# Kernel optimization log

Measured on AMD Instinct MI355X. Metric: run time of the kernel, lower is better.

## Reference

```python
import jax, jax.numpy as jnp
import numpy as np
from jax.scipy.linalg import expm

B, S, D_H, D_C = 8, 1024, 64, 3

def setup_inputs() -> dict:
    key = jax.random.key(0)
    k1, k2, k3 = jax.random.split(key, 3)
    x = jax.random.normal(k1, (B, S, D_H), dtype=jnp.float32)
    r_grid = jax.random.uniform(k2, (B, S, D_C), dtype=jnp.float32)
    L_param = jax.random.normal(k3, (D_C, D_H, D_H), dtype=jnp.float32)
    P_sp = jnp.eye(D_H, dtype=jnp.float32)  # allow_mixing=False -> identity buffer
    return {"x": x, "r_grid": r_grid, "L_param": L_param, "P_sp": P_sp}

def reference(x, r_grid, L_param, P_sp):
    # skew-symmetrize each generator: L_k <- 0.5*(L_k - L_k^T)
    L_skew = 0.5 * (L_param - jnp.swapaxes(L_param, -1, -2))      # [d_c, d_h, d_h]
    # A_r[b,s] = sum_k r_grid[b,s,k] * L_skew[k]
    A_r = jnp.einsum('bsk,kij->bsij', r_grid, L_skew)             # [B, S, d_h, d_h]
    # batched matrix exponential over leading dims
    R_r = expm(A_r)                                               # [B, S, d_h, d_h]
    R_eff = R_r @ P_sp                                            # [B, S, d_h, d_h]
    x_out = jnp.einsum('bsij,bsj->bsi', R_eff, x)                 # [B, S, d_h]
    return x_out
```

## Files before the change

### kernel.cpp

```cpp
#include <hip/hip_runtime.h>


typedef _Float16 half8 __attribute__((ext_vector_type(8)));
typedef __fp16 fp16x2 __attribute__((ext_vector_type(2)));
typedef float float4t __attribute__((ext_vector_type(4)));

union H2U { fp16x2 h; unsigned u; };

__device__ __forceinline__ unsigned pkrtz2(float a, float b) {
    H2U v; v.h = __builtin_amdgcn_cvt_pkrtz(a, b); return v.u;
}
__device__ __forceinline__ float h2lo(unsigned u) { H2U v; v.u = u; return (float)v.h[0]; }
__device__ __forceinline__ float h2hi(unsigned u) { H2U v; v.u = u; return (float)v.h[1]; }

__global__ void liepe_prep(const float* __restrict__ L, _Float16* __restrict__ wsA)
{
    int t = blockIdx.x * 256 + threadIdx.x;
    if (t >= 1536) return;
    int l   = t & 63;
    int f   = t >> 6;
    int kt  = f & 1;
    int m   = (f >> 1) & 3;
    int gen = f >> 3;
    int i   = 16 * m + (l & 15);
    int kk0 = 32 * kt + 8 * (l >> 4);
    const float* Lg = L + gen * 4096;
    half8 hi, lo;
    #pragma unroll
    for (int j = 0; j < 8; ++j) {
        int kk = kk0 + j;
        float d = Lg[i * 64 + kk] - Lg[kk * 64 + i];
        _Float16 h = (_Float16)d;
        hi[j] = h;
        lo[j] = (_Float16)(d - (float)h);
    }
    *(half8*)(wsA + f * 512 + l * 8) = hi;
    *(half8*)(wsA + 12288 + f * 512 + l * 8) = lo;
}


#define PSTR 36

#define STAGE_AND_LOAD_B()                                                       \
  {                                                                              \
    unsigned h0 = pkrtz2(b1[0], b1[1]);                                          \
    unsigned h1 = pkrtz2(b1[2], b1[3]);                                          \
    unsigned l0 = pkrtz2(b1[0] - h2lo(h0), b1[1] - h2hi(h0));                    \
    unsigned l1 = pkrtz2(b1[2] - h2lo(h1), b1[3] - h2hi(h1));                    \
    const int di = 8 * w + 2 * g;                                                \
    *(uint2*)&stage[buf][0][c][di] = make_uint2(h0, h1);                         \
    *(uint2*)&stage[buf][1][c][di] = make_uint2(l0, l1);                         \
    __syncthreads();                                                             \
    _Pragma("unroll")                                                            \
    for (int kt = 0; kt < 2; ++kt) {                                             \
      Bh[kt] = *(const half8*)&stage[buf][0][c][16 * kt + 4 * g];                \
      Bl[kt] = *(const half8*)&stage[buf][1][c][16 * kt + 4 * g];                \
    }                                                                            \
    buf ^= 1;                                                                    \
  }

#define GEMM_COMBINE(TOUT)                                                       \
  {                                                                              \
    _Pragma("unroll")                                                            \
    for (int gen = 0; gen < 3; ++gen) {                                          \
      float q = (gen == 0) ? q0 : ((gen == 1) ? q1 : q2);                        \
      float4t ac0 = {0.f, 0.f, 0.f, 0.f};                                        \
      float4t ac1 = {0.f, 0.f, 0.f, 0.f};                                        \
      ac0 = __builtin_amdgcn_mfma_f32_16x16x32_f16(Ah[gen*2+0], Bh[0], ac0, 0, 0, 0); \
      ac1 = __builtin_amdgcn_mfma_f32_16x16x32_f16(Ah[gen*2+1], Bh[1], ac1, 0, 0, 0); \
      ac0 = __builtin_amdgcn_mfma_f32_16x16x32_f16(Ah[gen*2+0], Bl[0], ac0, 0, 0, 0); \
      ac1 = __builtin_amdgcn_mfma_f32_16x16x32_f16(Ah[gen*2+1], Bl[1], ac1, 0, 0, 0); \
      ac0 = __builtin_amdgcn_mfma_f32_16x16x32_f16(Al[gen*2+0], Bh[0], ac0, 0, 0, 0); \
      ac1 = __builtin_amdgcn_mfma_f32_16x16x32_f16(Al[gen*2+1], Bh[1], ac1, 0, 0, 0); \
      _Pragma("unroll")                                                          \
      for (int r4 = 0; r4 < 4; ++r4) {                                           \
        float sum = ac0[r4] + ac1[r4];                                           \
        if (gen == 0) TOUT[r4] = q * sum;                                        \
        else          TOUT[r4] = fmaf(q, sum, TOUT[r4]);                         \
      }                                                                          \
    }                                                                            \
  }

__global__ __launch_bounds__(256) void liepe_mfma(
    const float* __restrict__ x,
    const float* __restrict__ r_grid,
    const _Float16* __restrict__ wsA,
    float* __restrict__ out,
    int n_tokens)
{
    __shared__ __align__(16) unsigned stage[2][2][16][PSTR];

    const int lane = threadIdx.x & 63;
    const int w    = threadIdx.x >> 6;
    const int c    = lane & 15;
    const int g    = lane >> 4;

    int tok = blockIdx.x * 16 + c;
    if (tok >= n_tokens) tok = n_tokens - 1;

    half8 Ah[6], Al[6];
    #pragma unroll
    for (int gen = 0; gen < 3; ++gen) {
        #pragma unroll
        for (int kt = 0; kt < 2; ++kt) {
            const int f = (gen * 4 + w) * 2 + kt;
            Ah[gen * 2 + kt] = *(const half8*)(wsA + f * 512 + lane * 8);
            Al[gen * 2 + kt] = *(const half8*)(wsA + 12288 + f * 512 + lane * 8);
        }
    }

    float xv[4];
    {
        float4 v = *(const float4*)(x + tok * 64 + 16 * w + 4 * g);
        xv[0] = v.x; xv[1] = v.y; xv[2] = v.z; xv[3] = v.w;
    }

    const float r0 = r_grid[tok * 3 + 0];
    const float r1 = r_grid[tok * 3 + 1];
    const float r2 = r_grid[tok * 3 + 2];
    const float sig2 = 0.5f * (r0 * r0 + r1 * r1 + r2 * r2);
    const float rho  = fmaf(17.3f, __builtin_sqrtf(sig2), 2.0f);
    const float inv_rho = 1.0f / rho;
    const int   M  = (int)rho + 14;
    const int   ms = M + 10;
    const float q0 = r0 * inv_rho, q1 = r1 * inv_rho, q2 = r2 * inv_rho;

    int maxM = M;
    #pragma unroll
    for (int off = 1; off < 64; off <<= 1)
        maxM = max(maxM, __shfl_xor(maxM, off));

    float jp = 0.f, jc = 0.f, N = 0.f;
    float b1[4] = {0.f, 0.f, 0.f, 0.f};
    float b2[4] = {0.f, 0.f, 0.f, 0.f};

    #pragma unroll 1
    for (int m = maxM + 10; m > maxM; --m) {
        bool sd = (m == ms);
        jc = sd ? 1e-12f : jc;
        jp = sd ? 0.f : jp;
        N  = sd ? (((m & 1) == 0) ? 2e-12f : 0.f) : N;
        float s = (jc > 1.0f) ? __builtin_amdgcn_rcpf(jc) : 1.0f;
        jc *= s; jp *= s; N *= s;
        float jm = fmaf((2.f * (float)m) * inv_rho, jc, -jp);
        jp = jc; jc = jm;
        int mm = m - 1;
        if ((mm & 1) == 0) N += (mm > 0) ? (jm + jm) : jm;
    }

    half8 Bh[2], Bl[2];
    int buf = 0;

    #pragma unroll 1
    for (int m = maxM; m >= 1; --m) {
        bool sd = (m == ms);
        jc = sd ? 1e-12f : jc;
        jp = sd ? 0.f : jp;
        N  = sd ? (((m & 1) == 0) ? 2e-12f : 0.f) : N;

        float s = (jc > 1.0f) ? __builtin_amdgcn_rcpf(jc) : 1.0f;
        jc *= s; jp *= s; N *= s;
        #pragma unroll
        for (int i = 0; i < 4; ++i) { b1[i] *= s; b2[i] *= s; }

        STAGE_AND_LOAD_B();

        float t[4];
        GEMM_COMBINE(t);

        float cf = (m <= M) ? (jc + jc) : 0.f;
        #pragma unroll
        for (int i = 0; i < 4; ++i) {
            float bn = fmaf(cf, xv[i], t[i] + b2[i]);
            b2[i] = b1[i];
            b1[i] = bn;
        }

        float jm = fmaf((2.f * (float)m) * inv_rho, jc, -jp);
        jp = jc; jc = jm;
        int mm = m - 1;
        if ((mm & 1) == 0) N += (mm > 0) ? (jm + jm) : jm;
    }

    {
        STAGE_AND_LOAD_B();
        float t[4];
        GEMM_COMBINE(t);
        float4 v;
        float y0 = fmaf(jc, xv[0], t[0] + b2[0]);
        float y1 = fmaf(jc, xv[1], t[1] + b2[1]);
        float y2 = fmaf(jc, xv[2], t[2] + b2[2]);
        float y3 = fmaf(jc, xv[3], t[3] + b2[3]);
        v.x = (y0 - 0.5f * t[0]) / N;
        v.y = (y1 - 0.5f * t[1]) / N;
        v.z = (y2 - 0.5f * t[2]) / N;
        v.w = (y3 - 0.5f * t[3]) / N;
        *(float4*)(out + tok * 64 + 16 * w + 4 * g) = v;
    }
}

extern "C" void kernel_launch(void* const* d_in, const int* in_sizes, int n_in,
                              void* d_out, int out_size, void* d_ws, size_t ws_size,
                              hipStream_t stream) {
    const float* x = (const float*)d_in[0];
    const float* r = (const float*)d_in[1];
    const float* L = (const float*)d_in[2];
    float* out = (float*)d_out;
    _Float16* wsA = (_Float16*)d_ws;

    int n_tokens = in_sizes[0] / 64;

    liepe_prep<<<6, 256, 0, stream>>>(L, wsA);

    int nwg = (n_tokens + 15) / 16;
    liepe_mfma<<<nwg, 256, 0, stream>>>(x, r, wsA, out, n_tokens);
}
```

Baseline: 32.11 us.

## Process two token groups per workgroup to interleave independent recurrences

Each workgroup now handles 32 tokens as two independent 16-token groups. Their Clenshaw/Miller recurrences and MFMA chains are interleaved so one barrier per step serves both groups, and MFMA latency of one group can hide behind the other. This halves the workgroup count (256 blocks for 8192 tokens) and raises register pressure, with waves_per_eu capped at 2. The shared maxM now spans 32 tokens, so some tokens may run extra iterations.

```diff
diff --git a/kernel.cpp b/kernel.cpp
--- a/kernel.cpp
+++ b/kernel.cpp
@@ -41,62 +41,122 @@
 
 #define PSTR 36
 
-#define STAGE_AND_LOAD_B()                                                       \
-  {                                                                              \
-    unsigned h0 = pkrtz2(b1[0], b1[1]);                                          \
-    unsigned h1 = pkrtz2(b1[2], b1[3]);                                          \
-    unsigned l0 = pkrtz2(b1[0] - h2lo(h0), b1[1] - h2hi(h0));                    \
-    unsigned l1 = pkrtz2(b1[2] - h2lo(h1), b1[3] - h2hi(h1));                    \
-    const int di = 8 * w + 2 * g;                                                \
-    *(uint2*)&stage[buf][0][c][di] = make_uint2(h0, h1);                         \
-    *(uint2*)&stage[buf][1][c][di] = make_uint2(l0, l1);                         \
-    __syncthreads();                                                             \
-    _Pragma("unroll")                                                            \
-    for (int kt = 0; kt < 2; ++kt) {                                             \
-      Bh[kt] = *(const half8*)&stage[buf][0][c][16 * kt + 4 * g];                \
-      Bl[kt] = *(const half8*)&stage[buf][1][c][16 * kt + 4 * g];                \
-    }                                                                            \
-    buf ^= 1;                                                                    \
+#define STAGE_B(G, B1)                                                        \
+  {                                                                           \
+    unsigned h0 = pkrtz2(B1[0], B1[1]);                                       \
+    unsigned h1 = pkrtz2(B1[2], B1[3]);                                       \
+    unsigned l0 = pkrtz2(B1[0] - h2lo(h0), B1[1] - h2hi(h0));                 \
+    unsigned l1 = pkrtz2(B1[2] - h2lo(h1), B1[3] - h2hi(h1));                 \
+    const int di = 8 * w + 2 * g;                                             \
+    *(uint2*)&stage[G][buf][0][c][di] = make_uint2(h0, h1);                   \
+    *(uint2*)&stage[G][buf][1][c][di] = make_uint2(l0, l1);                   \
   }
 
-#define GEMM_COMBINE(TOUT)                                                       \
-  {                                                                              \
-    _Pragma("unroll")                                                            \
-    for (int gen = 0; gen < 3; ++gen) {                                          \
-      float q = (gen == 0) ? q0 : ((gen == 1) ? q1 : q2);                        \
-      float4t ac0 = {0.f, 0.f, 0.f, 0.f};                                        \
-      float4t ac1 = {0.f, 0.f, 0.f, 0.f};                                        \
-      ac0 = __builtin_amdgcn_mfma_f32_16x16x32_f16(Ah[gen*2+0], Bh[0], ac0, 0, 0, 0); \
-      ac1 = __builtin_amdgcn_mfma_f32_16x16x32_f16(Ah[gen*2+1], Bh[1], ac1, 0, 0, 0); \
-      ac0 = __builtin_amdgcn_mfma_f32_16x16x32_f16(Ah[gen*2+0], Bl[0], ac0, 0, 0, 0); \
-      ac1 = __builtin_amdgcn_mfma_f32_16x16x32_f16(Ah[gen*2+1], Bl[1], ac1, 0, 0, 0); \
-      ac0 = __builtin_amdgcn_mfma_f32_16x16x32_f16(Al[gen*2+0], Bh[0], ac0, 0, 0, 0); \
-      ac1 = __builtin_amdgcn_mfma_f32_16x16x32_f16(Al[gen*2+1], Bh[1], ac1, 0, 0, 0); \
-      _Pragma("unroll")                                                          \
-      for (int r4 = 0; r4 < 4; ++r4) {                                           \
-        float sum = ac0[r4] + ac1[r4];                                           \
-        if (gen == 0) TOUT[r4] = q * sum;                                        \
-        else          TOUT[r4] = fmaf(q, sum, TOUT[r4]);                         \
-      }                                                                          \
-    }                                                                            \
+#define LOAD_B(G, BH, BL)                                                     \
+  {                                                                           \
+    _Pragma("unroll")                                                         \
+    for (int kt = 0; kt < 2; ++kt) {                                          \
+      BH[kt] = *(const half8*)&stage[G][buf][0][c][16 * kt + 4 * g];          \
+      BL[kt] = *(const half8*)&stage[G][buf][1][c][16 * kt + 4 * g];          \
+    }                                                                         \
   }
 
-__global__ __launch_bounds__(256) void liepe_mfma(
+#define GEMM_COMBINE(BH, BL, Q0, Q1, Q2, TOUT)                                \
+  {                                                                           \
+    _Pragma("unroll")                                                         \
+    for (int gen = 0; gen < 3; ++gen) {                                       \
+      float q = (gen == 0) ? Q0 : ((gen == 1) ? Q1 : Q2);                     \
+      float4t ac0 = {0.f, 0.f, 0.f, 0.f};                                     \
+      float4t ac1 = {0.f, 0.f, 0.f, 0.f};                                     \
+      ac0 = __builtin_amdgcn_mfma_f32_16x16x32_f16(Ah[gen*2+0], BH[0], ac0, 0, 0, 0); \
+      ac1 = __builtin_amdgcn_mfma_f32_16x16x32_f16(Ah[gen*2+1], BH[1], ac1, 0, 0, 0); \
+      ac0 = __builtin_amdgcn_mfma_f32_16x16x32_f16(Ah[gen*2+0], BL[0], ac0, 0, 0, 0); \
+      ac1 = __builtin_amdgcn_mfma_f32_16x16x32_f16(Ah[gen*2+1], BL[1], ac1, 0, 0, 0); \
+      ac0 = __builtin_amdgcn_mfma_f32_16x16x32_f16(Al[gen*2+0], BH[0], ac0, 0, 0, 0); \
+      ac1 = __builtin_amdgcn_mfma_f32_16x16x32_f16(Al[gen*2+1], BH[1], ac1, 0, 0, 0); \
+      _Pragma("unroll")                                                       \
+      for (int r4 = 0; r4 < 4; ++r4) {                                        \
+        float sum = ac0[r4] + ac1[r4];                                        \
+        if (gen == 0) TOUT[r4] = q * sum;                                     \
+        else          TOUT[r4] = fmaf(q, sum, TOUT[r4]);                      \
+      }                                                                       \
+    }                                                                         \
+  }
+
+#define SCALAR_PRE(S)                                                         \
+  { bool sd = (m == ms##S);                                                   \
+    jc##S = sd ? 1e-12f : jc##S;                                              \
+    jp##S = sd ? 0.f : jp##S;                                                 \
+    N##S  = sd ? (((m & 1) == 0) ? 2e-12f : 0.f) : N##S;                      \
+    float s = (jc##S > 1.0f) ? __builtin_amdgcn_rcpf(jc##S) : 1.0f;           \
+    jc##S *= s; jp##S *= s; N##S *= s;                                        \
+    _Pragma("unroll")                                                         \
+    for (int i = 0; i < 4; ++i) { b1##S[i] *= s; b2##S[i] *= s; } }
+
+#define SCALAR_POST(S, T)                                                     \
+  { float cf = (m <= M##S) ? (jc##S + jc##S) : 0.f;                           \
+    _Pragma("unroll")                                                         \
+    for (int i = 0; i < 4; ++i) {                                             \
+      float bn = fmaf(cf, xv##S[i], T[i] + b2##S[i]);                         \
+      b2##S[i] = b1##S[i]; b1##S[i] = bn; }                                   \
+    float jm = fmaf((2.f * (float)m) * inv##S, jc##S, -jp##S);                \
+    jp##S = jc##S; jc##S = jm;                                                \
+    int mm = m - 1;                                                           \
+    if ((mm & 1) == 0) N##S += (mm > 0) ? (jm + jm) : jm; }
+
+#define MILLER_DESC(S)                                                        \
+  { bool sd = (m == ms##S);                                                   \
+    jc##S = sd ? 1e-12f : jc##S;                                              \
+    jp##S = sd ? 0.f : jp##S;                                                 \
+    N##S  = sd ? (((m & 1) == 0) ? 2e-12f : 0.f) : N##S;                      \
+    float s = (jc##S > 1.0f) ? __builtin_amdgcn_rcpf(jc##S) : 1.0f;           \
+    jc##S *= s; jp##S *= s; N##S *= s;                                        \
+    float jm = fmaf((2.f * (float)m) * inv##S, jc##S, -jp##S);                \
+    jp##S = jc##S; jc##S = jm;                                                \
+    int mm = m - 1;                                                           \
+    if ((mm & 1) == 0) N##S += (mm > 0) ? (jm + jm) : jm; }
+
+#define INIT_GROUP(S, TOK)                                                    \
+    float xv##S[4];                                                           \
+    {                                                                         \
+        float4 v = *(const float4*)(x + (TOK) * 64 + 16 * w + 4 * g);         \
+        xv##S[0] = v.x; xv##S[1] = v.y; xv##S[2] = v.z; xv##S[3] = v.w;       \
+    }                                                                         \
+    const float r0##S = r_grid[(TOK) * 3 + 0];                                \
+    const float r1##S = r_grid[(TOK) * 3 + 1];                                \
+    const float r2##S = r_grid[(TOK) * 3 + 2];                                \
+    const float sig##S = 0.5f * (r0##S*r0##S + r1##S*r1##S + r2##S*r2##S);    \
+    const float rho##S = fmaf(17.3f, __builtin_sqrtf(sig##S), 2.0f);          \
+    const float inv##S = 1.0f / rho##S;                                       \
+    const int   M##S   = (int)rho##S + 14;                                    \
+    const int   ms##S  = M##S + 10;                                           \
+    const float q0##S = r0##S * inv##S;                                       \
+    const float q1##S = r1##S * inv##S;                                       \
+    const float q2##S = r2##S * inv##S;                                       \
+    float jp##S = 0.f, jc##S = 0.f, N##S = 0.f;                               \
+    float b1##S[4] = {0.f, 0.f, 0.f, 0.f};                                    \
+    float b2##S[4] = {0.f, 0.f, 0.f, 0.f};
+
+__global__ __launch_bounds__(256)
+__attribute__((amdgpu_waves_per_eu(1, 2)))
+void liepe_mfma(
     const float* __restrict__ x,
     const float* __restrict__ r_grid,
     const _Float16* __restrict__ wsA,
     float* __restrict__ out,
     int n_tokens)
 {
-    __shared__ __align__(16) unsigned stage[2][2][16][PSTR];
+    __shared__ __align__(16) unsigned stage[2][2][2][16][PSTR];
 
     const int lane = threadIdx.x & 63;
     const int w    = threadIdx.x >> 6;
     const int c    = lane & 15;
     const int g    = lane >> 4;
 
-    int tok = blockIdx.x * 16 + c;
-    if (tok >= n_tokens) tok = n_tokens - 1;
+    int tok0 = blockIdx.x * 32 + c;
+    int tok1 = blockIdx.x * 32 + 16 + c;
+    if (tok0 >= n_tokens) tok0 = n_tokens - 1;
+    if (tok1 >= n_tokens) tok1 = n_tokens - 1;
 
     half8 Ah[6], Al[6];
     #pragma unroll
@@ -109,93 +169,67 @@
         }
     }
 
-    float xv[4];
-    {
-        float4 v = *(const float4*)(x + tok * 64 + 16 * w + 4 * g);
-        xv[0] = v.x; xv[1] = v.y; xv[2] = v.z; xv[3] = v.w;
-    }
-
-    const float r0 = r_grid[tok * 3 + 0];
-    const float r1 = r_grid[tok * 3 + 1];
-    const float r2 = r_grid[tok * 3 + 2];
-    const float sig2 = 0.5f * (r0 * r0 + r1 * r1 + r2 * r2);
-    const float rho  = fmaf(17.3f, __builtin_sqrtf(sig2), 2.0f);
-    const float inv_rho = 1.0f / rho;
-    const int   M  = (int)rho + 14;
-    const int   ms = M + 10;
-    const float q0 = r0 * inv_rho, q1 = r1 * inv_rho, q2 = r2 * inv_rho;
-
-    int maxM = M;
+    INIT_GROUP(A, tok0)
+    INIT_GROUP(B, tok1)
+
+    int maxM = (MA > MB) ? MA : MB;
     #pragma unroll
     for (int off = 1; off < 64; off <<= 1)
         maxM = max(maxM, __shfl_xor(maxM, off));
 
-    float jp = 0.f, jc = 0.f, N = 0.f;
-    float b1[4] = {0.f, 0.f, 0.f, 0.f};
-    float b2[4] = {0.f, 0.f, 0.f, 0.f};
-
     #pragma unroll 1
     for (int m = maxM + 10; m > maxM; --m) {
-        bool sd = (m == ms);
-        jc = sd ? 1e-12f : jc;
-        jp = sd ? 0.f : jp;
-        N  = sd ? (((m & 1) == 0) ? 2e-12f : 0.f) : N;
-        float s = (jc > 1.0f) ? __builtin_amdgcn_rcpf(jc) : 1.0f;
-        jc *= s; jp *= s; N *= s;
-        float jm = fmaf((2.f * (float)m) * inv_rho, jc, -jp);
-        jp = jc; jc = jm;
-        int mm = m - 1;
-        if ((mm & 1) == 0) N += (mm > 0) ? (jm + jm) : jm;
-    }
-
-    half8 Bh[2], Bl[2];
+        MILLER_DESC(A)
+        MILLER_DESC(B)
+    }
+
+    half8 BhA[2], BlA[2], BhB[2], BlB[2];
     int buf = 0;
 
     #pragma unroll 1
     for (int m = maxM; m >= 1; --m) {
-        bool sd = (m == ms);
-        jc = sd ? 1e-12f : jc;
-        jp = sd ? 0.f : jp;
-        N  = sd ? (((m & 1) == 0) ? 2e-12f : 0.f) : N;
-
-        float s = (jc > 1.0f) ? __builtin_amdgcn_rcpf(jc) : 1.0f;
-        jc *= s; jp *= s; N *= s;
-        #pragma unroll
-        for (int i = 0; i < 4; ++i) { b1[i] *= s; b2[i] *= s; }
-
-        STAGE_AND_LOAD_B();
-
-        float t[4];
-        GEMM_COMBINE(t);
-
-        float cf = (m <= M) ? (jc + jc) : 0.f;
-        #pragma unroll
-        for (int i = 0; i < 4; ++i) {
-            float bn = fmaf(cf, xv[i], t[i] + b2[i]);
-            b2[i] = b1[i];
-            b1[i] = bn;
-        }
-
-        float jm = fmaf((2.f * (float)m) * inv_rho, jc, -jp);
-        jp = jc; jc = jm;
-        int mm = m - 1;
-        if ((mm & 1) == 0) N += (mm > 0) ? (jm + jm) : jm;
+        SCALAR_PRE(A)
+        SCALAR_PRE(B)
+
+        STAGE_B(0, b1A)
+        STAGE_B(1, b1B)
+        __syncthreads();
+        LOAD_B(0, BhA, BlA)
+        LOAD_B(1, BhB, BlB)
+
+        float tA[4], tB[4];
+        GEMM_COMBINE(BhA, BlA, q0A, q1A, q2A, tA)
+        GEMM_COMBINE(BhB, BlB, q0B, q1B, q2B, tB)
+
+        SCALAR_POST(A, tA)
+        SCALAR_POST(B, tB)
+        buf ^= 1;
     }
 
     {
-        STAGE_AND_LOAD_B();
-        float t[4];
-        GEMM_COMBINE(t);
+        STAGE_B(0, b1A)
+        STAGE_B(1, b1B)
+        __syncthreads();
+        LOAD_B(0, BhA, BlA)
+        LOAD_B(1, BhB, BlB)
+
+        float tA[4], tB[4];
+        GEMM_COMBINE(BhA, BlA, q0A, q1A, q2A, tA)
+        GEMM_COMBINE(BhB, BlB, q0B, q1B, q2B, tB)
+
         float4 v;
-        float y0 = fmaf(jc, xv[0], t[0] + b2[0]);
-        float y1 = fmaf(jc, xv[1], t[1] + b2[1]);
-        float y2 = fmaf(jc, xv[2], t[2] + b2[2]);
-        float y3 = fmaf(jc, xv[3], t[3] + b2[3]);
-        v.x = (y0 - 0.5f * t[0]) / N;
-        v.y = (y1 - 0.5f * t[1]) / N;
-        v.z = (y2 - 0.5f * t[2]) / N;
-        v.w = (y3 - 0.5f * t[3]) / N;
-        *(float4*)(out + tok * 64 + 16 * w + 4 * g) = v;
+        v.x = (fmaf(jcA, xvA[0], tA[0] + b2A[0]) - 0.5f * tA[0]) / NA;
+        v.y = (fmaf(jcA, xvA[1], tA[1] + b2A[1]) - 0.5f * tA[1]) / NA;
+        v.z = (fmaf(jcA, xvA[2], tA[2] + b2A[2]) - 0.5f * tA[2]) / NA;
+        v.w = (fmaf(jcA, xvA[3], tA[3] + b2A[3]) - 0.5f * tA[3]) / NA;
+        *(float4*)(out + tok0 * 64 + 16 * w + 4 * g) = v;
+
+        float4 u;
+        u.x = (fmaf(jcB, xvB[0], tB[0] + b2B[0]) - 0.5f * tB[0]) / NB;
+        u.y = (fmaf(jcB, xvB[1], tB[1] + b2B[1]) - 0.5f * tB[1]) / NB;
+        u.z = (fmaf(jcB, xvB[2], tB[2] + b2B[2]) - 0.5f * tB[2]) / NB;
+        u.w = (fmaf(jcB, xvB[3], tB[3] + b2B[3]) - 0.5f * tB[3]) / NB;
+        *(float4*)(out + tok1 * 64 + 16 * w + 4 * g) = u;
     }
 }
 
@@ -212,6 +246,6 @@
 
     liepe_prep<<<6, 256, 0, stream>>>(L, wsA);
 
-    int nwg = (n_tokens + 15) / 16;
+    int nwg = (n_tokens + 31) / 32;
     liepe_mfma<<<nwg, 256, 0, stream>>>(x, r, wsA, out, n_tokens);
 }
```

Result: slower. 37.66 us (+17.3%).
